# Optimization experiments

Hardware: AMD Instinct MI355X
Metric: run time of the kernel (lower is better)

The kernel has to match this reference:

```python
import jax, jax.numpy as jnp
import numpy as np

B, N, DIM = 4, 2048, 1024
HEADS, DH = 16, 64
INNER = HEADS * DH
SCALE = 8.0
EPS = 1e-5


def setup_inputs() -> dict:
    key = jax.random.key(0)
    ks = jax.random.split(key, 8)
    x = jax.random.normal(ks[0], (B, N, DIM), dtype=jnp.float32)
    context_mask = jax.random.bernoulli(ks[1], 0.9, (B, N))
    gamma = jnp.ones((DIM,), dtype=jnp.float32)
    null_kv = jax.random.normal(ks[2], (2, HEADS, 1, DH), dtype=jnp.float32)
    Wq = jax.random.normal(ks[3], (DIM, INNER), dtype=jnp.float32) * 0.02
    Wkv = jax.random.normal(ks[4], (DIM, 2 * INNER), dtype=jnp.float32) * 0.02
    # q_scale init: scale / dim_head**-0.5 = 8 * sqrt(64) = 64
    q_scale = jnp.full((DH,), SCALE * (DH ** 0.5), dtype=jnp.float32)
    k_scale = jnp.ones((DH,), dtype=jnp.float32)
    Wout = jax.random.normal(ks[5], (INNER, DIM), dtype=jnp.float32) * 0.02
    return {"x": x, "context_mask": context_mask, "gamma": gamma,
            "null_kv": null_kv, "Wq": Wq, "Wkv": Wkv,
            "q_scale": q_scale, "k_scale": k_scale, "Wout": Wout}


def _l2norm(t):
    return t / jnp.sqrt(jnp.sum(t * t, axis=-1, keepdims=True) + 1e-12)


def reference(x, context_mask, gamma, null_kv, Wq, Wkv, q_scale, k_scale, Wout):
    b, n, _ = x.shape
    # LayerNorm (beta buffer is zeros)
    mu = jnp.mean(x, axis=-1, keepdims=True)
    var = jnp.mean((x - mu) ** 2, axis=-1, keepdims=True)
    xn = (x - mu) / jnp.sqrt(var + EPS) * gamma
    # projections
    q = (xn @ Wq).reshape(b, n, HEADS, DH)
    kv = xn @ Wkv
    k = kv[..., :INNER].reshape(b, n, HEADS, DH)
    v = kv[..., INNER:].reshape(b, n, HEADS, DH)
    # null kv token: [h,1,d] -> [b,1,h,d]
    nk = jnp.broadcast_to(null_kv[0].transpose(1, 0, 2)[None], (b, 1, HEADS, DH))
    nv = jnp.broadcast_to(null_kv[1].transpose(1, 0, 2)[None], (b, 1, HEADS, DH))
    k = jnp.concatenate([nk, k], axis=1)  # [b, n+1, h, d]
    v = jnp.concatenate([nv, v], axis=1)
    # cosine-sim attention with learned per-dim scales
    q = _l2norm(q) * q_scale
    k = _l2norm(k) * k_scale
    # bias from mask (padded True for null token)
    mask = jnp.pad(context_mask, ((0, 0), (1, 0)), constant_values=True)
    bias = jnp.where(mask, 0.0, -10000.0)[:, None, None, :]  # [b,1,1,n+1]
    # memory_efficient_attention applies 1/sqrt(dh) internally
    scores = jnp.einsum('bqhd,bkhd->bhqk', q, k) * (DH ** -0.5) + bias
    attn = jax.nn.softmax(scores, axis=-1)
    out = jnp.einsum('bhqk,bkhd->bqhd', attn, v).reshape(b, n, INNER)
    return out @ Wout
```

## Files before the change

kernel.cpp:

```cpp
#include <hip/hip_runtime.h>
#include <hip/hip_bf16.h>
#include <stdint.h>


using f32x4  = __attribute__((ext_vector_type(4))) float;
using bf16x8 = __attribute__((ext_vector_type(8))) __bf16;
using f16x8  = __attribute__((ext_vector_type(8))) _Float16;
using uintv4 = __attribute__((ext_vector_type(4))) unsigned int;

__device__ __forceinline__ float b2f(unsigned short u) {
    return __uint_as_float(((unsigned)u) << 16);
}
__device__ __forceinline__ unsigned short f2b(float f) {
    unsigned u = __float_as_uint(f);
    u += 0x7fffu + ((u >> 16) & 1u);
    return (unsigned short)(u >> 16);
}
__device__ __forceinline__ f32x4 mfma16(bf16x8 a, bf16x8 b, f32x4 c) {
    return __builtin_amdgcn_mfma_f32_16x16x32_bf16(a, b, c, 0, 0, 0);
}
__device__ __forceinline__ f32x4 mfma16h(f16x8 a, f16x8 b, f32x4 c) {
    return __builtin_amdgcn_mfma_f32_16x16x32_f16(a, b, c, 0, 0, 0);
}
__device__ __forceinline__ unsigned pk16(float a, float b) {
    return __builtin_bit_cast(unsigned, __builtin_amdgcn_cvt_pkrtz(a, b));
}
__device__ __forceinline__ void gl_lds16(const void* g, void* l) {
    __builtin_amdgcn_global_load_lds(
        (const __attribute__((address_space(1))) unsigned int*)g,
        (__attribute__((address_space(3))) unsigned int*)l, 16, 0, 0);
}

__global__ __launch_bounds__(256) void transpose_f2b(
    const float* __restrict__ in, unsigned short* __restrict__ out,
    int R, int C)
{
    __shared__ unsigned short t[32][33];
    int tx = threadIdx.x, ty = threadIdx.y;
    int c = blockIdx.x * 32 + tx;
#pragma unroll
    for (int i = 0; i < 4; ++i) {
        int r = blockIdx.y * 32 + ty + i * 8;
        t[ty + i * 8][tx] = f2b(in[(size_t)r * C + c]);
    }
    __syncthreads();
    int r2 = blockIdx.y * 32 + tx;
#pragma unroll
    for (int i = 0; i < 4; ++i) {
        int c2 = blockIdx.x * 32 + ty + i * 8;
        out[(size_t)c2 * R + r2] = t[tx][ty + i * 8];
    }
}

__global__ __launch_bounds__(256) void ln_kernel(
    const float* __restrict__ x, const float* __restrict__ gamma,
    unsigned short* __restrict__ xn)
{
    int row = blockIdx.x, tid = threadIdx.x;
    int wave = tid >> 6, lane = tid & 63;
    float4 raw = *(const float4*)(x + ((size_t)row << 10) + (tid << 2));
    float v[4] = { raw.x, raw.y, raw.z, raw.w };
    float s  = v[0] + v[1] + v[2] + v[3];
    float s2 = v[0]*v[0] + v[1]*v[1] + v[2]*v[2] + v[3]*v[3];
#pragma unroll
    for (int off = 1; off < 64; off <<= 1) {
        s  += __shfl_xor(s, off);
        s2 += __shfl_xor(s2, off);
    }
    __shared__ float ps[4], ps2[4], sh[2];
    if (lane == 0) { ps[wave] = s; ps2[wave] = s2; }
    __syncthreads();
    if (tid == 0) {
        float S  = ps[0] + ps[1] + ps[2] + ps[3];
        float S2 = ps2[0] + ps2[1] + ps2[2] + ps2[3];
        float mu  = S * (1.f / 1024.f);
        float var = S2 * (1.f / 1024.f) - mu * mu;
        sh[0] = mu; sh[1] = rsqrtf(var + 1e-5f);
    }
    __syncthreads();
    float mu = sh[0], rstd = sh[1];
    float4 g4 = *(const float4*)(gamma + (tid << 2));
    float g[4] = { g4.x, g4.y, g4.z, g4.w };
    unsigned short o[4];
#pragma unroll
    for (int i = 0; i < 4; ++i) o[i] = f2b((v[i] - mu) * rstd * g[i]);
    uint2 out;
    out.x = (unsigned)o[0] | ((unsigned)o[1] << 16);
    out.y = (unsigned)o[2] | ((unsigned)o[3] << 16);
    *(uint2*)(xn + ((size_t)row << 10) + (tid << 2)) = out;
}

template<int MODE>
__global__ __launch_bounds__(256, 2) void gemm_bt(
    const unsigned short* __restrict__ A, const unsigned short* __restrict__ Bt,
    void* __restrict__ Cout, const float* __restrict__ scale,
    unsigned short* __restrict__ Vout,
    int M, int N, int K, int ldc)
{
    __shared__ __bf16 As[128 * 32];
    __shared__ __bf16 Bs[128 * 32];
    int tid = threadIdx.x, lane = tid & 63, wave = tid >> 6;
    int quad = lane >> 4, l15 = lane & 15;
    int m0 = blockIdx.y * 128, n0 = blockIdx.x * 128;
    int wm = (wave & 1) * 64, wn = (wave >> 1) * 64;
    f32x4 acc[4][4] = {};

    const int srow = wave * 32 + (lane >> 2);
    const int scol = (lane & 3) << 3;
    const unsigned short* gA = A  + (size_t)(m0 + srow) * K + scol;
    const unsigned short* gB = Bt + (size_t)(n0 + srow) * K + scol;
    __bf16* lA0 = &As[(wave * 32) * 32];
    __bf16* lA1 = &As[(wave * 32 + 16) * 32];
    __bf16* lB0 = &Bs[(wave * 32) * 32];
    __bf16* lB1 = &Bs[(wave * 32 + 16) * 32];
    const size_t rstep = (size_t)16 * K;

    for (int k0 = 0; k0 < K; k0 += 32) {
        gl_lds16(gA,         lA0);
        gl_lds16(gA + rstep, lA1);
        gl_lds16(gB,         lB0);
        gl_lds16(gB + rstep, lB1);
        gA += 32; gB += 32;
        __syncthreads();
        bf16x8 af[4], bfv[4];
#pragma unroll
        for (int i = 0; i < 4; ++i)
            af[i] = *(const bf16x8*)&As[(wm + i * 16 + l15) * 32 + quad * 8];
#pragma unroll
        for (int j = 0; j < 4; ++j)
            bfv[j] = *(const bf16x8*)&Bs[(wn + j * 16 + l15) * 32 + quad * 8];
#pragma unroll
        for (int i = 0; i < 4; ++i)
#pragma unroll
            for (int j = 0; j < 4; ++j)
                acc[i][j] = mfma16(af[i], bfv[j], acc[i][j]);
        __syncthreads();
    }

    if (MODE == 2) {
#pragma unroll
        for (int i = 0; i < 4; ++i)
#pragma unroll
            for (int j = 0; j < 4; ++j) {
                int row = m0 + wm + i * 16 + quad * 4;
                int col = n0 + wn + j * 16 + l15;
                size_t base = (size_t)row * ldc + col;
#pragma unroll
                for (int r = 0; r < 4; ++r)
                    ((float*)Cout)[base + (size_t)r * ldc] = acc[i][j][r];
            }
        return;
    }

    const bool isv = (MODE == 1) && ((n0 + wn) >= 1024);
    if (MODE == 1 && isv) {
        int hv = (n0 + wn - 1024) >> 6;
#pragma unroll
        for (int i = 0; i < 4; ++i)
#pragma unroll
            for (int r = 0; r < 4; ++r) {
                int tok = m0 + wm + i * 16 + quad * 4 + r;
                int b = tok >> 11;
                int col = (tok & 2047) + 1;
                size_t rowb = (size_t)(((b << 4) + hv) << 6);
#pragma unroll
                for (int j = 0; j < 4; ++j) {
                    float v = acc[i][j][r];
                    Vout[(rowb + j * 16 + l15) * 2056 + col] =
                        __builtin_bit_cast(unsigned short, (_Float16)v);
                }
            }
        return;
    }

    float sc[4];
#pragma unroll
    for (int j = 0; j < 4; ++j) {
        float s = scale[j * 16 + l15];
        sc[j] = (MODE == 0) ? s * (0.125f * 1.44269504088896f) : s;
    }
#pragma unroll
    for (int i = 0; i < 4; ++i)
#pragma unroll
        for (int r = 0; r < 4; ++r) {
            float ss = 0.f;
#pragma unroll
            for (int j = 0; j < 4; ++j) ss += acc[i][j][r] * acc[i][j][r];
            ss += __shfl_xor(ss, 1); ss += __shfl_xor(ss, 2);
            ss += __shfl_xor(ss, 4); ss += __shfl_xor(ss, 8);
            float mul = rsqrtf(ss + 1e-12f);
            size_t rowbase = (size_t)(m0 + wm + i * 16 + quad * 4 + r) * ldc
                           + n0 + wn + l15;
#pragma unroll
            for (int j = 0; j < 4; ++j) {
                float v = acc[i][j][r];
                ((unsigned short*)Cout)[rowbase + j * 16] = f2b(v * mul * sc[j]);
            }
        }
}

__global__ __launch_bounds__(256) void nullkv_kernel(
    const float* __restrict__ null_kv, const float* __restrict__ k_scale,
    unsigned short* __restrict__ knull, unsigned short* __restrict__ Vt)
{
    int wave = threadIdx.x >> 6, lane = threadIdx.x & 63;
    int h = blockIdx.x * 4 + wave;
    int idx = (h << 6) + lane;
    float kvl = null_kv[idx];
    float ss = kvl * kvl;
#pragma unroll
    for (int off = 1; off < 64; off <<= 1) ss += __shfl_xor(ss, off);
    knull[idx] = f2b(kvl * rsqrtf(ss + 1e-12f) * k_scale[lane]);
    unsigned short vn =
        __builtin_bit_cast(unsigned short, (_Float16)null_kv[1024 + idx]);
#pragma unroll
    for (int b = 0; b < 4; ++b)
        Vt[((size_t)(((b << 4) + h) << 6) + lane) * 2056] = vn;
    int t = blockIdx.x * 256 + threadIdx.x;
    uintv4 z = { 0u, 0u, 0u, 0u };
#pragma unroll
    for (int rr = 0; rr < 4; ++rr) {
        size_t row = (size_t)t * 4 + rr;
        *(uintv4*)(Vt + row * 2056 + 2048) = z;
    }
}

__global__ __launch_bounds__(256, 3) void attn_kernel(
    const unsigned short* __restrict__ qn,
    const unsigned short* __restrict__ kvK,
    const unsigned short* __restrict__ knull,
    const unsigned short* __restrict__ Vt,
    const int* __restrict__ mask,
    unsigned short* __restrict__ ao)
{
    __shared__ __bf16    Kt[2][64 * 64];
    __shared__ _Float16  Vl[2][64 * 64];
    __shared__ __align__(16) float biasLds[2][64];

    const int tid = threadIdx.x, lane = tid & 63, wave = tid >> 6;
    const int quad = lane >> 4, l15 = lane & 15;
    const int bh = blockIdx.x;
    const int b = bh >> 4, h = bh & 15;
    const int mbase = blockIdx.y * 128 + wave * 32;
    const size_t rowoff = (size_t)b * 2048;

    bf16x8 qf[2][2];
#pragma unroll
    for (int rg = 0; rg < 2; ++rg)
#pragma unroll
        for (int ks = 0; ks < 2; ++ks)
            qf[rg][ks] = *(const bf16x8*)
                &qn[((rowoff + mbase + rg * 16 + l15) << 10) + (h << 6) + ks * 32 + quad * 8];

    const int t8  = lane >> 3;
    const int w7  = lane & 7;
    const int ksc = (w7 ^ t8) << 3;
    const size_t vrow0 = ((size_t)bh << 6);

    auto kIssue = [&](int nt, int buf) {
#pragma unroll
        for (int p = 0; p < 2; ++p) {
            int r = wave * 16 + p * 8 + t8;
            int T = ((r >> 5) << 5) | (((r >> 2) & 3) << 3)
                  | (((r >> 4) & 1) << 2) | (r & 3);
            int j = (nt << 6) + T;
            int jr = j - 1; if (jr > 2047) jr = 2047;
            const unsigned short* src = (j == 0)
                ? knull + (h << 6) + ksc
                : kvK + ((rowoff + (size_t)jr) << 10) + (h << 6) + ksc;
            gl_lds16(src, &Kt[buf][(wave * 16 + p * 8) * 64]);
        }
    };
    auto vIssue = [&](int nt, int buf) {
#pragma unroll
        for (int p = 0; p < 2; ++p) {
            int d = wave * 16 + p * 8 + t8;
            int gsrc = (nt << 3) + (w7 ^ t8);
            if (gsrc > 256) gsrc = 256;
            const unsigned short* src = Vt + (vrow0 + d) * 2056 + (gsrc << 3);
            gl_lds16(src, &Vl[buf][(wave * 16 + p * 8) * 64]);
        }
    };
    auto biasFor = [&](int nt) -> float {
        int j = (nt << 6) + tid;
        float bv = -512.f;
        if (j == 0 || (j <= 2048 && mask[b * 2048 + j - 1] != 0)) bv = 0.f;
        return bv;
    };

    f32x4 O[2][4] = {};
    float rs[2] = {0.f, 0.f};

    kIssue(0, 0);
    vIssue(0, 0);
    float bcur = biasFor(0);

    for (int nt = 0; nt < 33; ++nt) {
        const int buf = nt & 1;
        if (tid < 64) biasLds[buf][tid] = bcur;
        __syncthreads();
        if (nt < 32) {
            kIssue(nt + 1, buf ^ 1);
            vIssue(nt + 1, buf ^ 1);
            bcur = biasFor(nt + 1);
        }

#pragma unroll
        for (int g = 0; g < 2; ++g) {
            float4 b0 = *(const float4*)&biasLds[buf][(g << 5) + (quad << 3)];
            float4 b1 = *(const float4*)&biasLds[buf][(g << 5) + (quad << 3) + 4];
            f32x4 s[2][2];
#pragma unroll
            for (int rg = 0; rg < 2; ++rg) {
                s[rg][0] = f32x4{ b0.x, b0.y, b0.z, b0.w };
                s[rg][1] = f32x4{ b1.x, b1.y, b1.z, b1.w };
            }
#pragma unroll
            for (int t = 0; t < 2; ++t) {
                const __bf16* kb = &Kt[buf][((g * 2 + t) * 16 + l15) * 64];
                bf16x8 k0 = *(const bf16x8*)&kb[(quad ^ (l15 & 7)) << 3];
                bf16x8 k1 = *(const bf16x8*)&kb[((4 + quad) ^ (l15 & 7)) << 3];
#pragma unroll
                for (int rg = 0; rg < 2; ++rg) {
                    s[rg][t] = mfma16(k0, qf[rg][0], s[rg][t]);
                    s[rg][t] = mfma16(k1, qf[rg][1], s[rg][t]);
                }
            }
            f16x8 vf8[4];
#pragma unroll
            for (int dt = 0; dt < 4; ++dt)
                vf8[dt] = *(const f16x8*)
                    &Vl[buf][(dt * 16 + l15) * 64
                             + ((((g << 2) + quad) ^ (l15 & 7)) << 3)];
#pragma unroll
            for (int rg = 0; rg < 2; ++rg) {
                float e0 = __builtin_amdgcn_exp2f(s[rg][0][0]);
                float e1 = __builtin_amdgcn_exp2f(s[rg][0][1]);
                float e2 = __builtin_amdgcn_exp2f(s[rg][0][2]);
                float e3 = __builtin_amdgcn_exp2f(s[rg][0][3]);
                float e4 = __builtin_amdgcn_exp2f(s[rg][1][0]);
                float e5 = __builtin_amdgcn_exp2f(s[rg][1][1]);
                float e6 = __builtin_amdgcn_exp2f(s[rg][1][2]);
                float e7 = __builtin_amdgcn_exp2f(s[rg][1][3]);
                rs[rg] += ((e0 + e1) + (e2 + e3)) + ((e4 + e5) + (e6 + e7));
                uintv4 pu = { pk16(e0, e1), pk16(e2, e3),
                              pk16(e4, e5), pk16(e6, e7) };
                f16x8 p = __builtin_bit_cast(f16x8, pu);
#pragma unroll
                for (int dt = 0; dt < 4; ++dt)
                    O[rg][dt] = mfma16h(p, vf8[dt], O[rg][dt]);
            }
        }
    }

#pragma unroll
    for (int rg = 0; rg < 2; ++rg) {
        rs[rg] += __shfl_xor(rs[rg], 16);
        rs[rg] += __shfl_xor(rs[rg], 32);
    }
#pragma unroll
    for (int rg = 0; rg < 2; ++rg) {
        float inv[4];
#pragma unroll
        for (int r = 0; r < 4; ++r)
            inv[r] = 1.f / __shfl(rs[rg], quad * 4 + r);
#pragma unroll
        for (int dt = 0; dt < 4; ++dt) {
            size_t base = ((rowoff + mbase + rg * 16 + quad * 4) << 10)
                        + (h << 6) + dt * 16 + l15;
#pragma unroll
            for (int r = 0; r < 4; ++r)
                ao[base + ((size_t)r << 10)] = f2b(O[rg][dt][r] * inv[r]);
        }
    }
}

extern "C" void kernel_launch(void* const* d_in, const int* in_sizes, int n_in,
                              void* d_out, int out_size, void* d_ws, size_t ws_size,
                              hipStream_t stream)
{
    const float* x       = (const float*)d_in[0];
    const int*   mask    = (const int*)d_in[1];
    const float* gamma   = (const float*)d_in[2];
    const float* null_kv = (const float*)d_in[3];
    const float* Wq      = (const float*)d_in[4];
    const float* Wkv     = (const float*)d_in[5];
    const float* q_scale = (const float*)d_in[6];
    const float* k_scale = (const float*)d_in[7];
    const float* Wout    = (const float*)d_in[8];

    char* ws = (char*)d_ws;
    const size_t VTG_OFF  = (size_t)48u << 20;
    const size_t VTG_SIZE = (size_t)4096 * 4112;
    unsigned short* xn    = (unsigned short*)(ws);
    unsigned short* ao    = xn;
    unsigned short* q     = (unsigned short*)(ws + ((size_t)16u << 20));
    unsigned short* kvK   = (unsigned short*)(ws + ((size_t)32u << 20));
    unsigned short* VtG   = (unsigned short*)(ws + VTG_OFF);
    unsigned short* WqT   = (unsigned short*)(ws + VTG_OFF + VTG_SIZE - ((size_t)2u << 20));
    unsigned short* WkvT  = (unsigned short*)(ws + VTG_OFF + VTG_SIZE);
    unsigned short* WoutT = (unsigned short*)(ws + VTG_OFF + VTG_SIZE + ((size_t)4u << 20));
    unsigned short* knull = (unsigned short*)(ws + VTG_OFF + VTG_SIZE + ((size_t)6u << 20));

    dim3 tb(32, 8);
    transpose_f2b<<<dim3(32, 32), tb, 0, stream>>>(Wq,   WqT,   1024, 1024);
    transpose_f2b<<<dim3(64, 32), tb, 0, stream>>>(Wkv,  WkvT,  1024, 2048);
    transpose_f2b<<<dim3(32, 32), tb, 0, stream>>>(Wout, WoutT, 1024, 1024);

    ln_kernel<<<8192, 256, 0, stream>>>(x, gamma, xn);

    gemm_bt<0><<<dim3(8, 64),  256, 0, stream>>>(xn, WqT, q, q_scale, nullptr,
                                                 8192, 1024, 1024, 1024);
    nullkv_kernel<<<4, 256, 0, stream>>>(null_kv, k_scale, knull, VtG);

    gemm_bt<1><<<dim3(16, 64), 256, 0, stream>>>(xn, WkvT, kvK, k_scale, VtG,
                                                 8192, 2048, 1024, 1024);

    attn_kernel<<<dim3(64, 16), 256, 0, stream>>>(q, kvK, knull, VtG, mask, ao);

    gemm_bt<2><<<dim3(8, 64), 256, 0, stream>>>(ao, WoutT, d_out, nullptr, nullptr,
                                                8192, 1024, 1024, 1024);
}
```

Before: 313.6 us.

## Stage V transpose through LDS and move null token to end of key sequence

```diff
diff --git a/kernel.cpp b/kernel.cpp
--- a/kernel.cpp
+++ b/kernel.cpp
@@ -15,6 +15,9 @@
     unsigned u = __float_as_uint(f);
     u += 0x7fffu + ((u >> 16) & 1u);
     return (unsigned short)(u >> 16);
+}
+__device__ __forceinline__ unsigned short f2h(float f) {
+    return __builtin_bit_cast(unsigned short, (_Float16)f);
 }
 __device__ __forceinline__ f32x4 mfma16(bf16x8 a, bf16x8 b, f32x4 c) {
     return __builtin_amdgcn_mfma_f32_16x16x32_bf16(a, b, c, 0, 0, 0);
@@ -152,25 +155,37 @@
         return;
     }
 
-    const bool isv = (MODE == 1) && ((n0 + wn) >= 1024);
-    if (MODE == 1 && isv) {
-        int hv = (n0 + wn - 1024) >> 6;
-#pragma unroll
-        for (int i = 0; i < 4; ++i)
-#pragma unroll
-            for (int r = 0; r < 4; ++r) {
-                int tok = m0 + wm + i * 16 + quad * 4 + r;
-                int b = tok >> 11;
-                int col = (tok & 2047) + 1;
-                size_t rowb = (size_t)(((b << 4) + hv) << 6);
+    if constexpr (MODE == 1) {
+        const bool isv = (n0 + wn) >= 1024;
+        if (isv) {
+            __shared__ unsigned short Vx[4][64 * 64];
+            unsigned short* tileL = Vx[wave];
+            int hv = (n0 + wn - 1024) >> 6;
+            int bidx = m0 >> 11;
+            int tok0w = (m0 + wm) & 2047;
+            size_t vbase = (size_t)((((bidx << 4) + hv) << 6)) * 2056;
+#pragma unroll
+            for (int i = 0; i < 4; ++i)
 #pragma unroll
                 for (int j = 0; j < 4; ++j) {
-                    float v = acc[i][j][r];
-                    Vout[(rowb + j * 16 + l15) * 2056 + col] =
-                        __builtin_bit_cast(unsigned short, (_Float16)v);
+                    int d = j * 16 + l15;
+                    int tk = (i * 16 + quad * 4) ^ ((d & 7) << 3);
+                    unsigned u01 = (unsigned)f2h(acc[i][j][0])
+                                 | ((unsigned)f2h(acc[i][j][1]) << 16);
+                    unsigned u23 = (unsigned)f2h(acc[i][j][2])
+                                 | ((unsigned)f2h(acc[i][j][3]) << 16);
+                    *(unsigned*)&tileL[d * 64 + tk]     = u01;
+                    *(unsigned*)&tileL[d * 64 + tk + 2] = u23;
                 }
-            }
-        return;
+#pragma unroll
+            for (int rr = 0; rr < 16; ++rr) {
+                int d = rr * 4 + quad;
+                uint2 val = *(const uint2*)
+                    &tileL[d * 64 + ((l15 * 4) ^ ((d & 7) << 3))];
+                *(uint2*)(Vout + vbase + (size_t)d * 2056 + tok0w + l15 * 4) = val;
+            }
+            return;
+        }
     }
 
     float sc[4];
@@ -211,17 +226,17 @@
 #pragma unroll
     for (int off = 1; off < 64; off <<= 1) ss += __shfl_xor(ss, off);
     knull[idx] = f2b(kvl * rsqrtf(ss + 1e-12f) * k_scale[lane]);
-    unsigned short vn =
-        __builtin_bit_cast(unsigned short, (_Float16)null_kv[1024 + idx]);
+    unsigned short vn = f2h(null_kv[1024 + idx]);
 #pragma unroll
     for (int b = 0; b < 4; ++b)
-        Vt[((size_t)(((b << 4) + h) << 6) + lane) * 2056] = vn;
+        Vt[((size_t)(((b << 4) + h) << 6) + lane) * 2056 + 2048] = vn;
     int t = blockIdx.x * 256 + threadIdx.x;
-    uintv4 z = { 0u, 0u, 0u, 0u };
 #pragma unroll
     for (int rr = 0; rr < 4; ++rr) {
         size_t row = (size_t)t * 4 + rr;
-        *(uintv4*)(Vt + row * 2056 + 2048) = z;
+#pragma unroll
+        for (int c = 0; c < 7; ++c)
+            Vt[row * 2056 + 2049 + c] = 0;
     }
 }
 
@@ -257,52 +272,64 @@
     const int ksc = (w7 ^ t8) << 3;
     const size_t vrow0 = ((size_t)bh << 6);
 
-    auto kIssue = [&](int nt, int buf) {
-#pragma unroll
-        for (int p = 0; p < 2; ++p) {
-            int r = wave * 16 + p * 8 + t8;
-            int T = ((r >> 5) << 5) | (((r >> 2) & 3) << 3)
-                  | (((r >> 4) & 1) << 2) | (r & 3);
-            int j = (nt << 6) + T;
-            int jr = j - 1; if (jr > 2047) jr = 2047;
-            const unsigned short* src = (j == 0)
-                ? knull + (h << 6) + ksc
-                : kvK + ((rowoff + (size_t)jr) << 10) + (h << 6) + ksc;
-            gl_lds16(src, &Kt[buf][(wave * 16 + p * 8) * 64]);
-        }
+    const int r0v = wave * 16 + t8;
+    const int r1v = wave * 16 + 8 + t8;
+    auto Tof = [](int r) {
+        return ((r >> 5) << 5) | (((r >> 2) & 3) << 3)
+             | (((r >> 4) & 1) << 2) | (r & 3);
     };
-    auto vIssue = [&](int nt, int buf) {
-#pragma unroll
-        for (int p = 0; p < 2; ++p) {
-            int d = wave * 16 + p * 8 + t8;
-            int gsrc = (nt << 3) + (w7 ^ t8);
-            if (gsrc > 256) gsrc = 256;
-            const unsigned short* src = Vt + (vrow0 + d) * 2056 + (gsrc << 3);
-            gl_lds16(src, &Vl[buf][(wave * 16 + p * 8) * 64]);
-        }
+    const int T0 = Tof(r0v), T1 = Tof(r1v);
+
+    const unsigned short* kp0 = kvK + ((rowoff + T0) << 10) + (h << 6) + ksc;
+    const unsigned short* kp1 = kvK + ((rowoff + T1) << 10) + (h << 6) + ksc;
+    const unsigned short* vp0 = Vt + (vrow0 + r0v) * 2056 + ((w7 ^ t8) << 3);
+    const unsigned short* vp1 = Vt + (vrow0 + r1v) * 2056 + ((w7 ^ t8) << 3);
+
+    auto issueFast = [&](int bf) {
+        gl_lds16(kp0, &Kt[bf][(wave * 16) * 64]);
+        gl_lds16(kp1, &Kt[bf][(wave * 16 + 8) * 64]);
+        gl_lds16(vp0, &Vl[bf][(wave * 16) * 64]);
+        gl_lds16(vp1, &Vl[bf][(wave * 16 + 8) * 64]);
+        kp0 += 65536; kp1 += 65536;
+        vp0 += 64; vp1 += 64;
+    };
+    auto issue32 = [&](int bf) {
+        const unsigned short* kc =
+            kvK + ((rowoff + 2047) << 10) + (h << 6) + ksc;
+        const unsigned short* s0 = (T0 == 0) ? knull + (h << 6) + ksc : kc;
+        gl_lds16(s0, &Kt[bf][(wave * 16) * 64]);
+        gl_lds16(kc, &Kt[bf][(wave * 16 + 8) * 64]);
+        gl_lds16(Vt + (vrow0 + r0v) * 2056 + 2048, &Vl[bf][(wave * 16) * 64]);
+        gl_lds16(Vt + (vrow0 + r1v) * 2056 + 2048, &Vl[bf][(wave * 16 + 8) * 64]);
     };
     auto biasFor = [&](int nt) -> float {
-        int j = (nt << 6) + tid;
+        int j = (nt << 6) + lane;
         float bv = -512.f;
-        if (j == 0 || (j <= 2048 && mask[b * 2048 + j - 1] != 0)) bv = 0.f;
+        if (j < 2048) { if (mask[(b << 11) + j] != 0) bv = 0.f; }
+        else if (j == 2048) bv = 0.f;
         return bv;
     };
 
+    const uintv4 onesu = { 0x3c003c00u, 0x3c003c00u, 0x3c003c00u, 0x3c003c00u };
+    const f16x8 ones = __builtin_bit_cast(f16x8, onesu);
+
     f32x4 O[2][4] = {};
-    float rs[2] = {0.f, 0.f};
-
-    kIssue(0, 0);
-    vIssue(0, 0);
-    float bcur = biasFor(0);
+    f32x4 rsacc[2] = {};
+
+    issueFast(0);
+    float bcur = 0.f;
+    if (wave == 0) bcur = biasFor(0);
 
     for (int nt = 0; nt < 33; ++nt) {
         const int buf = nt & 1;
-        if (tid < 64) biasLds[buf][tid] = bcur;
+        if (wave == 0) biasLds[buf][lane] = bcur;
         __syncthreads();
-        if (nt < 32) {
-            kIssue(nt + 1, buf ^ 1);
-            vIssue(nt + 1, buf ^ 1);
-            bcur = biasFor(nt + 1);
+        if (nt < 31) {
+            issueFast(buf ^ 1);
+            if (wave == 0) bcur = biasFor(nt + 1);
+        } else if (nt == 31) {
+            issue32(buf ^ 1);
+            if (wave == 0) bcur = biasFor(32);
         }
 
 #pragma unroll
@@ -342,10 +369,10 @@
                 float e5 = __builtin_amdgcn_exp2f(s[rg][1][1]);
                 float e6 = __builtin_amdgcn_exp2f(s[rg][1][2]);
                 float e7 = __builtin_amdgcn_exp2f(s[rg][1][3]);
-                rs[rg] += ((e0 + e1) + (e2 + e3)) + ((e4 + e5) + (e6 + e7));
                 uintv4 pu = { pk16(e0, e1), pk16(e2, e3),
                               pk16(e4, e5), pk16(e6, e7) };
                 f16x8 p = __builtin_bit_cast(f16x8, pu);
+                rsacc[rg] = mfma16h(p, ones, rsacc[rg]);
 #pragma unroll
                 for (int dt = 0; dt < 4; ++dt)
                     O[rg][dt] = mfma16h(p, vf8[dt], O[rg][dt]);
@@ -355,15 +382,9 @@
 
 #pragma unroll
     for (int rg = 0; rg < 2; ++rg) {
-        rs[rg] += __shfl_xor(rs[rg], 16);
-        rs[rg] += __shfl_xor(rs[rg], 32);
-    }
-#pragma unroll
-    for (int rg = 0; rg < 2; ++rg) {
         float inv[4];
 #pragma unroll
-        for (int r = 0; r < 4; ++r)
-            inv[r] = 1.f / __shfl(rs[rg], quad * 4 + r);
+        for (int r = 0; r < 4; ++r) inv[r] = 1.f / rsacc[rg][r];
 #pragma unroll
         for (int dt = 0; dt < 4; ++dt) {
             size_t base = ((rowoff + mbase + rg * 16 + quad * 4) << 10)
```

After: 299.8 us. -4.4%, faster.
